# Optimization experiments

Measured on AMD Instinct MI355X. Metric: run time of the kernel, lower is better.

Reference implementation:

```python
import jax, jax.numpy as jnp
import numpy as np

NUM_HEADS = 8
EPS = 1e-12  # torch F.normalize default eps


def conv1x1(x, w):
    # x: [b,c,h,w], w: [o,c]
    return jnp.einsum('bchw,oc->bohw', x, w)


def dwconv3x3(x, w):
    # depthwise 3x3, w: [c,1,3,3]
    return jax.lax.conv_general_dilated(
        x, w, window_strides=(1, 1), padding=((1, 1), (1, 1)),
        dimension_numbers=('NCHW', 'OIHW', 'NCHW'),
        feature_group_count=x.shape[1])


def l2norm(x):
    n = jnp.sqrt(jnp.sum(x * x, axis=-1, keepdims=True))
    return x / jnp.maximum(n, EPS)


def channel_attn(q, k, v, temperature, b, c, h, w):
    hd = c // NUM_HEADS
    q = l2norm(q.reshape(b, NUM_HEADS, hd, h * w))
    k = l2norm(k.reshape(b, NUM_HEADS, hd, h * w))
    v = v.reshape(b, NUM_HEADS, hd, h * w)
    attn = jnp.einsum('bndl,bnel->bnde', q, k) * temperature  # [b,nh,hd,hd]
    attn = jax.nn.softmax(attn, axis=-1)
    out = jnp.einsum('bnde,bnel->bndl', attn, v)
    return out.reshape(b, c, h, w)


def fdfp(x, w1, w2, h, w):
    xf = jnp.fft.rfft2(x, norm='ortho')  # over last two axes
    xfreq = jnp.concatenate([xf.real, xf.imag], axis=1)
    xfreq = conv1x1(xfreq, w1)
    xfreq = jax.nn.gelu(xfreq, approximate=False)
    xfreq = conv1x1(xfreq, w2)
    c2 = xfreq.shape[1] // 2
    xc = jax.lax.complex(xfreq[:, :c2], xfreq[:, c2:])
    return jnp.fft.irfft2(xc, s=(h, w), norm='ortho')


def setup_inputs() -> dict:
    key = jax.random.key(0)
    ks = jax.random.split(key, 10)
    dim = 192
    b, h, w = 4, 128, 128
    s = 0.05
    return {
        'x': jax.random.normal(ks[0], (b, dim, h, w), jnp.float32),
        'w_qkv1': jax.random.normal(ks[1], (3 * dim, dim), jnp.float32) * s,
        'w_qkv1_dw': jax.random.normal(ks[2], (3 * dim, 1, 3, 3), jnp.float32) * s,
        'w_proj1': jax.random.normal(ks[3], (dim, dim), jnp.float32) * s,
        'w_fdfp1': jax.random.normal(ks[4], (2 * dim, 2 * dim), jnp.float32) * s,
        'w_fdfp2': jax.random.normal(ks[5], (2 * dim, 2 * dim), jnp.float32) * s,
        'w_kv2': jax.random.normal(ks[6], (2 * dim, dim), jnp.float32) * s,
        'w_kv2_dw': jax.random.normal(ks[7], (2 * dim, 1, 3, 3), jnp.float32) * s,
        'w_proj2': jax.random.normal(ks[8], (dim, dim), jnp.float32) * s,
        'temperature': jnp.ones((NUM_HEADS, 1, 1), jnp.float32),
    }


def reference(x, w_qkv1, w_qkv1_dw, w_proj1, w_fdfp1, w_fdfp2,
              w_kv2, w_kv2_dw, w_proj2, temperature):
    b, c, h, w = x.shape
    # Stage 1: spatial-domain transposed (channel) attention
    qkv1 = dwconv3x3(conv1x1(x, w_qkv1), w_qkv1_dw)
    q1, k1, v1 = jnp.split(qkv1, 3, axis=1)
    out1 = channel_attn(q1, k1, v1, temperature, b, c, h, w)
    out1 = conv1x1(out1, w_proj1)
    # Stage 2: frequency-domain query, spatial K/V from stage-1 output
    q2 = fdfp(x, w_fdfp1, w_fdfp2, h, w)
    kv2 = dwconv3x3(conv1x1(out1, w_kv2), w_kv2_dw)
    k2, v2 = jnp.split(kv2, 2, axis=1)
    out2 = channel_attn(q2, k2, v2, temperature, b, c, h, w)
    out2 = conv1x1(out2, w_proj2)
    return out2
```

## Files before the change

### kernel.cpp

```cpp
#include <hip/hip_runtime.h>
#include <math.h>

typedef _Float16 half_t;
typedef half_t h8v __attribute__((ext_vector_type(8)));
typedef half_t h4v __attribute__((ext_vector_type(4)));
typedef float f32x4 __attribute__((ext_vector_type(4)));

namespace {
constexpr int DIMC = 192;
constexpr int NB = 4;
constexpr int HH = 128, WW = 128;
constexpr int HW = HH * WW;
constexpr int NH = 8, HD = 24;
constexpr int FP = 80;
constexpr long LT_PART = 128L * 192 * FP;
constexpr long LT_B    = 2 * LT_PART;
constexpr long LT_ROW  = 192L * FP;
constexpr long XB  = 192L * HW;
constexpr long CB0 = 0;
constexpr long CB1 = 15728640;
constexpr long OFF_T1 = 37748736;
constexpr long OFF_Q2 = 50331648;
constexpr long OFF_S  = 62914560;
constexpr long OFF_KT = 0;
constexpr long OFF_KF = 25165824;
constexpr long OFF_O2 = 0;
constexpr int  GSL = 64;
constexpr long SM_INVQ1 = OFF_S;
constexpr long SM_INVK1 = OFF_S + 768;
constexpr long SM_INVQ2 = OFF_S + 1536;
constexpr long SM_INVK2 = OFF_S + 2304;
constexpr long SM_ATT   = OFF_S + 3072;
constexpr long H0       = OFF_S + 168960;
constexpr long H_WQKV = H0;
constexpr long H_WF   = H0 + 55296;
constexpr long H_W1   = H0 + 92160;
constexpr long H_W2   = H0 + 165888;
constexpr long H_PRJ  = H0 + 239616;
constexpr long H_B2   = H0 + 258048;
constexpr long H_B3   = H0 + 290816;
constexpr long H_B1T  = H0 + 323584;
constexpr long H_B4T  = H0 + 333824;
constexpr float PI2 = 6.283185307179586476f;
}

__global__ void cvt16_k(const float* __restrict__ in, half_t* __restrict__ o, int n) {
    int i = blockIdx.x * 256 + threadIdx.x;
    if (i < n) o[i] = (half_t)in[i];
}
__global__ void initB1t_k(half_t* __restrict__ B) {
    int idx = blockIdx.x * 256 + threadIdx.x;
    if (idx >= 160 * 128) return;
    int j = idx / 128, k = idx % 128;
    float v = 0.f;
    if (j < 65) v = cosf(PI2 * ((k * j) & 127) / 128.f) * (1.f / 128.f);
    else if (j >= 80 && j < 145) v = -sinf(PI2 * ((k * (j - 80)) & 127) / 128.f) * (1.f / 128.f);
    B[idx] = (half_t)v;
}
__global__ void initB2h_k(half_t* __restrict__ B) {
    int idx = blockIdx.x * 256 + threadIdx.x;
    int m = idx >> 8, cin = idx & 255;
    int pd = m >> 7, ky = m & 127;
    int ps = cin >> 7, y = cin & 127;
    float c, s; sincosf(PI2 * ((ky * y) & 127) / 128.f, &s, &c);
    float v = (pd == 0) ? (ps == 0 ? c : s) : (ps == 0 ? -s : c);
    B[idx] = (half_t)v;
}
__global__ void initB3h_k(half_t* __restrict__ B) {
    int idx = blockIdx.x * 256 + threadIdx.x;
    int m = idx >> 8, cin = idx & 255;
    int pd = m >> 7, y = m & 127;
    int ps = cin >> 7, ky = cin & 127;
    float c, s; sincosf(PI2 * ((y * ky) & 127) / 128.f, &s, &c);
    float v = (pd == 0) ? (ps == 0 ? c : -s) : (ps == 0 ? s : c);
    B[idx] = (half_t)v;
}
__global__ void initB4t_k(half_t* __restrict__ B) {
    int idx = blockIdx.x * 256 + threadIdx.x;
    if (idx >= 128 * 160) return;
    int j = idx / 160, k = idx % 160;
    float v = 0.f;
    if (k < 80) {
        if (k == 0) v = 1.f / 128.f;
        else if (k < 64) v = 2.f * cosf(PI2 * ((k * j) & 127) / 128.f) / 128.f;
        else if (k == 64) v = cosf(PI2 * ((64 * j) & 127) / 128.f) / 128.f;
    } else {
        int kx = k - 80;
        if (kx >= 1 && kx < 64) v = -2.f * sinf(PI2 * ((kx * j) & 127) / 128.f) / 128.f;
    }
    B[idx] = (half_t)v;
}
__global__ void fusew_k(const float* __restrict__ wkv, const float* __restrict__ wproj,
                        half_t* __restrict__ wf) {
    int o = blockIdx.x, c = threadIdx.x;
    float acc = 0.f;
    for (int m = 0; m < 192; ++m) acc += wkv[o * 192 + m] * wproj[m * 192 + c];
    wf[o * 192 + c] = (half_t)acc;
}

template<int PFOLD, int GELU>
__global__ __launch_bounds__(256) void k2m(
    const half_t* __restrict__ W16, int Cin,
    const float* __restrict__ X, long xBatch, int iSplit, long iLo, long iHi,
    float* __restrict__ out, long oBatch, int oSplit, long oLo, long oHi) {
    __shared__ __align__(16) half_t Wh[64 * 40];
    __shared__ __align__(16) half_t Xh[256 * 40];
    const int t = threadIdx.x;
    const int o0 = blockIdx.x * 64;
    const long p0 = (long)blockIdx.y * 256;
    const long xb = (long)blockIdx.z * xBatch;
    const long ob = (long)blockIdx.z * oBatch;
    const int lane = t & 63, wv = t >> 6;
    const int fr = lane & 15, fg = lane >> 4;
    const int so = t >> 2, scg = (t & 3) * 8;
    f32x4 acc[4][4];
#pragma unroll
    for (int m = 0; m < 4; ++m)
#pragma unroll
        for (int n = 0; n < 4; ++n) acc[m][n] = {0.f, 0.f, 0.f, 0.f};
    long pa;
    {
        long p = p0 + t;
        if (PFOLD) { long q = p / 80; pa = q * LT_ROW + (p - q * 80); } else pa = p;
    }
    for (int k0 = 0; k0 < Cin; k0 += 32) {
        __syncthreads();
        *(h8v*)&Wh[so * 40 + scg] =
            *(const h8v*)(W16 + (long)(o0 + so) * Cin + k0 + scg);
#pragma unroll
        for (int s = 0; s < 2; ++s) {
            int cb = k0 + s * 16;
            long rb = (cb < iSplit) ? (long)cb * iLo : (long)(cb - iSplit) * iLo + iHi;
            const float* g = X + xb + rb + pa;
            float v[16];
#pragma unroll
            for (int j = 0; j < 16; ++j) v[j] = g[(long)j * iLo];
            h8v h0, h1;
#pragma unroll
            for (int j = 0; j < 8; ++j) { h0[j] = (half_t)v[j]; h1[j] = (half_t)v[8 + j]; }
            *(h8v*)&Xh[t * 40 + s * 16] = h0;
            *(h8v*)&Xh[t * 40 + s * 16 + 8] = h1;
        }
        __syncthreads();
        h8v a[4], bb[4];
#pragma unroll
        for (int m = 0; m < 4; ++m) a[m] = *(const h8v*)&Wh[(m * 16 + fr) * 40 + fg * 8];
#pragma unroll
        for (int n = 0; n < 4; ++n) bb[n] = *(const h8v*)&Xh[(wv * 64 + n * 16 + fr) * 40 + fg * 8];
#pragma unroll
        for (int m = 0; m < 4; ++m)
#pragma unroll
            for (int n = 0; n < 4; ++n)
                acc[m][n] = __builtin_amdgcn_mfma_f32_16x16x32_f16(a[m], bb[n], acc[m][n], 0, 0, 0);
    }
    long pe[4];
#pragma unroll
    for (int n = 0; n < 4; ++n) {
        long p = p0 + wv * 64 + n * 16 + fr;
        if (PFOLD) { long q = p / 80; pe[n] = q * LT_ROW + (p - q * 80); } else pe[n] = p;
    }
#pragma unroll
    for (int m = 0; m < 4; ++m)
#pragma unroll
        for (int i = 0; i < 4; ++i) {
            int o = o0 + m * 16 + fg * 4 + i;
            long oadr = ob + ((o < oSplit) ? (long)o * oLo : (long)(o - oSplit) * oLo + oHi);
#pragma unroll
            for (int n = 0; n < 4; ++n) {
                float v = acc[m][n][i];
                if (GELU) v = 0.5f * v * (1.f + erff(v * 0.70710678118654752f));
                out[oadr + pe[n]] = v;
            }
        }
}

__global__ __launch_bounds__(256) void k2big(
    const half_t* __restrict__ B16,
    const float* __restrict__ X, float* __restrict__ out) {
    __shared__ __align__(16) half_t Xh[8 * 64 * 40];
    const int t = threadIdx.x;
    const long p0 = (long)blockIdx.x * 64;
    const long xb = (long)blockIdx.y * LT_B;
    const int lane = t & 63, wv = t >> 6;
    const int fr = lane & 15, fg = lane >> 4;
    {
        const int sp = t & 63;
        const int c0 = t >> 6;
        const float* gp = X + xb + p0 + sp;
#pragma unroll 8
        for (int j = 0; j < 64; ++j) {
            int ci = c0 + j * 4;
            long rb = (ci < 128) ? (long)ci * LT_ROW : (long)(ci - 128) * LT_ROW + LT_PART;
            Xh[((ci >> 5) * 64 + sp) * 40 + (ci & 31)] = (half_t)gp[rb];
        }
    }
    __syncthreads();
    f32x4 acc[4][4];
#pragma unroll
    for (int m = 0; m < 4; ++m)
#pragma unroll
        for (int n = 0; n < 4; ++n) acc[m][n] = {0.f, 0.f, 0.f, 0.f};
    for (int k0 = 0; k0 < 256; k0 += 32) {
        const int s = k0 >> 5;
        h8v a[4], bb[4];
#pragma unroll
        for (int m = 0; m < 4; ++m)
            a[m] = *(const h8v*)(B16 + (long)(wv * 64 + m * 16 + fr) * 256 + k0 + fg * 8);
#pragma unroll
        for (int n = 0; n < 4; ++n)
            bb[n] = *(const h8v*)&Xh[(s * 64 + n * 16 + fr) * 40 + fg * 8];
#pragma unroll
        for (int m = 0; m < 4; ++m)
#pragma unroll
            for (int n = 0; n < 4; ++n)
                acc[m][n] = __builtin_amdgcn_mfma_f32_16x16x32_f16(a[m], bb[n], acc[m][n], 0, 0, 0);
    }
#pragma unroll
    for (int m = 0; m < 4; ++m)
#pragma unroll
        for (int i = 0; i < 4; ++i) {
            int o = wv * 64 + m * 16 + fg * 4 + i;
            long oadr = xb + ((o < 128) ? (long)o * LT_ROW : (long)(o - 128) * LT_ROW + LT_PART);
#pragma unroll
            for (int n = 0; n < 4; ++n)
                out[oadr + p0 + n * 16 + fr] = acc[m][n][i];
        }
}

__global__ __launch_bounds__(512) void kff(
    const half_t* __restrict__ W1, const half_t* __restrict__ W2,
    const float* __restrict__ X, float* __restrict__ out) {
    __shared__ __align__(16) half_t Wh[384 * 40];
    __shared__ __align__(16) half_t Xh[64 * 40];
    __shared__ __align__(16) half_t Yh[64 * 392];
    const int t = threadIdx.x;
    const long p0 = (long)blockIdx.x * 64;
    const long xb = (long)blockIdx.y * LT_B;
    const int lane = t & 63, wv = t >> 6;
    const int fr = lane & 15, fg = lane >> 4;
    const int sp = t & 63;
    const int skb = (t >> 6) * 4;
    long pa;
    { long p = p0 + sp; long q = p / 80; pa = q * LT_ROW + (p - q * 80); }
    f32x4 acc[3][4];
#pragma unroll
    for (int m = 0; m < 3; ++m)
#pragma unroll
        for (int n = 0; n < 4; ++n) acc[m][n] = {0.f, 0.f, 0.f, 0.f};

    for (int k0 = 0; k0 < 384; k0 += 32) {
        __syncthreads();
#pragma unroll
        for (int r = 0; r < 3; ++r) {
            int task = t + r * 512;
            int o = task >> 2, kg = (task & 3) * 8;
            *(h8v*)&Wh[o * 40 + kg] = *(const h8v*)(W1 + (long)o * 384 + k0 + kg);
        }
        {
            int c0 = k0 + skb;
            long rb = (c0 < 192) ? (long)c0 * 80 : (long)(c0 - 192) * 80 + LT_PART;
            const float* g = X + xb + rb + pa;
            h4v h;
#pragma unroll
            for (int j = 0; j < 4; ++j) h[j] = (half_t)g[(long)j * 80];
            *(h4v*)&Xh[sp * 40 + skb] = h;
        }
        __syncthreads();
        h8v a[3], bb[4];
#pragma unroll
        for (int m = 0; m < 3; ++m) a[m] = *(const h8v*)&Wh[(wv * 48 + m * 16 + fr) * 40 + fg * 8];
#pragma unroll
        for (int n = 0; n < 4; ++n) bb[n] = *(const h8v*)&Xh[(n * 16 + fr) * 40 + fg * 8];
#pragma unroll
        for (int m = 0; m < 3; ++m)
#pragma unroll
            for (int n = 0; n < 4; ++n)
                acc[m][n] = __builtin_amdgcn_mfma_f32_16x16x32_f16(a[m], bb[n], acc[m][n], 0, 0, 0);
    }
#pragma unroll
    for (int m = 0; m < 3; ++m)
#pragma unroll
        for (int n = 0; n < 4; ++n) {
            int o4 = wv * 48 + m * 16 + fg * 4;
            int p = n * 16 + fr;
            h4v h;
#pragma unroll
            for (int i = 0; i < 4; ++i) {
                float v = acc[m][n][i];
                v = 0.5f * v * (1.f + erff(v * 0.70710678118654752f));
                h[i] = (half_t)v;
            }
            *(h4v*)&Yh[p * 392 + o4] = h;
        }
#pragma unroll
    for (int m = 0; m < 3; ++m)
#pragma unroll
        for (int n = 0; n < 4; ++n) acc[m][n] = {0.f, 0.f, 0.f, 0.f};

    for (int k0 = 0; k0 < 384; k0 += 32) {
        __syncthreads();
#pragma unroll
        for (int r = 0; r < 3; ++r) {
            int task = t + r * 512;
            int o = task >> 2, kg = (task & 3) * 8;
            *(h8v*)&Wh[o * 40 + kg] = *(const h8v*)(W2 + (long)o * 384 + k0 + kg);
        }
        __syncthreads();
        h8v a[3], bb[4];
#pragma unroll
        for (int m = 0; m < 3; ++m) a[m] = *(const h8v*)&Wh[(wv * 48 + m * 16 + fr) * 40 + fg * 8];
#pragma unroll
        for (int n = 0; n < 4; ++n) bb[n] = *(const h8v*)&Yh[(n * 16 + fr) * 392 + k0 + fg * 8];
#pragma unroll
        for (int m = 0; m < 3; ++m)
#pragma unroll
            for (int n = 0; n < 4; ++n)
                acc[m][n] = __builtin_amdgcn_mfma_f32_16x16x32_f16(a[m], bb[n], acc[m][n], 0, 0, 0);
    }
    long pe[4];
#pragma unroll
    for (int n = 0; n < 4; ++n) {
        long p = p0 + n * 16 + fr;
        long q = p / 80; pe[n] = q * LT_ROW + (p - q * 80);
    }
#pragma unroll
    for (int m = 0; m < 3; ++m)
#pragma unroll
        for (int i = 0; i < 4; ++i) {
            int o = wv * 48 + m * 16 + fg * 4 + i;
            long oadr = xb + ((o < 192) ? (long)o * 80 : (long)(o - 192) * 80 + LT_PART);
#pragma unroll
            for (int n = 0; n < 4; ++n) out[oadr + pe[n]] = acc[m][n][i];
        }
}

template<int NF, int NORM>
__global__ __launch_bounds__(256) void k1m(
    const float* __restrict__ A, long aBatch, long aC, long aRow, int aSplit, long aHiOff, int K,
    const uint* __restrict__ Bt32,
    float* __restrict__ out, long oBatch, long oC, long oRow, int oSplit, long oHiOff,
    float* __restrict__ inv) {
    __shared__ __align__(16) half_t Ah[128 * 40];
    __shared__ __align__(16) half_t Bh[160 * 40];
    const int t = threadIdx.x;
    const long ab = (long)blockIdx.z * aBatch + (long)blockIdx.x * aC;
    const long ob = (long)blockIdx.z * oBatch + (long)blockIdx.x * oC;
    const int N = NF * 32;
    const int lane = t & 63, wv = t >> 6;
    const int wm = wv >> 1, wn = wv & 1;
    const int fr = lane & 15, fg = lane >> 4;
    const int sr = t >> 1, shalf = t & 1;
    const int Kw = K >> 1;
    f32x4 acc[4][NF];
#pragma unroll
    for (int m = 0; m < 4; ++m)
#pragma unroll
        for (int n = 0; n < NF; ++n) acc[m][n] = {0.f, 0.f, 0.f, 0.f};
    for (int k0 = 0; k0 < K; k0 += 32) {
        __syncthreads();
        {
            int cb = k0 + shalf * 16;
            long rb = (cb < aSplit) ? (long)cb : (long)(cb - aSplit) + aHiOff;
            const float* g = A + ab + (long)sr * aRow + rb;
            float4 v0 = *(const float4*)g;
            float4 v1 = *(const float4*)(g + 4);
            float4 v2 = *(const float4*)(g + 8);
            float4 v3 = *(const float4*)(g + 12);
            h8v h0, h1;
            h0[0] = (half_t)v0.x; h0[1] = (half_t)v0.y; h0[2] = (half_t)v0.z; h0[3] = (half_t)v0.w;
            h0[4] = (half_t)v1.x; h0[5] = (half_t)v1.y; h0[6] = (half_t)v1.z; h0[7] = (half_t)v1.w;
            h1[0] = (half_t)v2.x; h1[1] = (half_t)v2.y; h1[2] = (half_t)v2.z; h1[3] = (half_t)v2.w;
            h1[4] = (half_t)v3.x; h1[5] = (half_t)v3.y; h1[6] = (half_t)v3.z; h1[7] = (half_t)v3.w;
            *(h8v*)&Ah[sr * 40 + shalf * 16] = h0;
            *(h8v*)&Ah[sr * 40 + shalf * 16 + 8] = h1;
        }
        for (int j = t; j < N * 16; j += 256) {
            int n = j >> 4, kw = j & 15;
            *(uint*)&Bh[n * 40 + kw * 2] = Bt32[(long)n * Kw + (k0 >> 1) + kw];
        }
        __syncthreads();
        h8v a[4], bb[NF];
#pragma unroll
        for (int m = 0; m < 4; ++m) a[m] = *(const h8v*)&Ah[(wm * 64 + m * 16 + fr) * 40 + fg * 8];
#pragma unroll
        for (int n = 0; n < NF; ++n) bb[n] = *(const h8v*)&Bh[(wn * NF * 16 + n * 16 + fr) * 40 + fg * 8];
#pragma unroll
        for (int m = 0; m < 4; ++m)
#pragma unroll
            for (int n = 0; n < NF; ++n)
                acc[m][n] = __builtin_amdgcn_mfma_f32_16x16x32_f16(a[m], bb[n], acc[m][n], 0, 0, 0);
    }
#pragma unroll
    for (int m = 0; m < 4; ++m)
#pragma unroll
        for (int i = 0; i < 4; ++i) {
            int r = wm * 64 + m * 16 + fg * 4 + i;
            float* orow = out + ob + (long)r * oRow;
#pragma unroll
            for (int n = 0; n < NF; ++n) {
                int j = wn * NF * 16 + n * 16 + fr;
                long jm = (j < oSplit) ? (long)j : (long)(j - oSplit) + oHiOff;
                orow[jm] = acc[m][n][i];
            }
        }
    if (NORM) {
        float ss = 0.f;
#pragma unroll
        for (int m = 0; m < 4; ++m)
#pragma unroll
            for (int n = 0; n < NF; ++n)
#pragma unroll
                for (int i = 0; i < 4; ++i) ss += acc[m][n][i] * acc[m][n][i];
        __syncthreads();
        float* red = (float*)Ah;
        red[t] = ss;
        __syncthreads();
        for (int st = 128; st > 0; st >>= 1) {
            if (t < st) red[t] += red[t + st];
            __syncthreads();
        }
        if (t == 0) inv[(long)blockIdx.z * 192 + blockIdx.x] = 1.f / fmaxf(sqrtf(red[0]), 1e-12f);
    }
}

__global__ __launch_bounds__(256) void dw3_k(
    const float* __restrict__ in, long inBatch,
    const float* __restrict__ w9,
    float* __restrict__ out, long outBatch,
    int normCnt, float* __restrict__ inv) {
    const int c = blockIdx.x, b = blockIdx.y;
    const int t = threadIdx.x;
    const float* ip = in + (long)b * inBatch + (long)c * HW;
    float* op = out + (long)b * outBatch + (long)c * HW;
    const float* wp = w9 + c * 9;
    const float w0 = wp[0], w1 = wp[1], w2 = wp[2];
    const float w3 = wp[3], w4 = wp[4], w5 = wp[5];
    const float w6 = wp[6], w7 = wp[7], w8 = wp[8];
    const int tx = t & 31;
    const int x0 = tx * 4;
    const int y0 = (t >> 5) * 16;
    const bool lx = (tx > 0), rx = (tx < 31);
    float Ar[6], Br[6], Cr[6];
#define LOADROW(Y, R) do { \
        const float* _p = ip + (Y) * 128 + x0; \
        float4 _v = *(const float4*)_p; \
        R[1] = _v.x; R[2] = _v.y; R[3] = _v.z; R[4] = _v.w; \
        R[0] = lx ? _p[-1] : 0.f; \
        R[5] = rx ? _p[4] : 0.f; } while (0)
    if (y0 == 0) { Ar[0]=Ar[1]=Ar[2]=Ar[3]=Ar[4]=Ar[5]=0.f; }
    else LOADROW(y0 - 1, Ar);
    LOADROW(y0, Br);
    float ss = 0.f;
#pragma unroll
    for (int i = 0; i < 16; ++i) {
        int y = y0 + i;
        if (y + 1 < 128) { LOADROW(y + 1, Cr); }
        else { Cr[0]=Cr[1]=Cr[2]=Cr[3]=Cr[4]=Cr[5]=0.f; }
        float o0 = Ar[0]*w0 + Ar[1]*w1 + Ar[2]*w2
                 + Br[0]*w3 + Br[1]*w4 + Br[2]*w5
                 + Cr[0]*w6 + Cr[1]*w7 + Cr[2]*w8;
        float o1 = Ar[1]*w0 + Ar[2]*w1 + Ar[3]*w2
                 + Br[1]*w3 + Br[2]*w4 + Br[3]*w5
                 + Cr[1]*w6 + Cr[2]*w7 + Cr[3]*w8;
        float o2 = Ar[2]*w0 + Ar[3]*w1 + Ar[4]*w2
                 + Br[2]*w3 + Br[3]*w4 + Br[4]*w5
                 + Cr[2]*w6 + Cr[3]*w7 + Cr[4]*w8;
        float o3 = Ar[3]*w0 + Ar[4]*w1 + Ar[5]*w2
                 + Br[3]*w3 + Br[4]*w4 + Br[5]*w5
                 + Cr[3]*w6 + Cr[4]*w7 + Cr[5]*w8;
        *(float4*)(op + y * 128 + x0) = make_float4(o0, o1, o2, o3);
        ss += o0*o0 + o1*o1 + o2*o2 + o3*o3;
#pragma unroll
        for (int j = 0; j < 6; ++j) { Ar[j] = Br[j]; Br[j] = Cr[j]; }
    }
#undef LOADROW
    if (normCnt > 0 && c < normCnt) {
        __shared__ float red[256];
        red[t] = ss;
        __syncthreads();
        for (int st = 128; st > 0; st >>= 1) {
            if (t < st) red[t] += red[t + st];
            __syncthreads();
        }
        if (t == 0) inv[(long)b * 192 + c] = 1.f / fmaxf(sqrtf(red[0]), 1e-12f);
    }
}

__global__ __launch_bounds__(576) void gramf_k(
    const float* __restrict__ q, long qB,
    const float* __restrict__ k, long kB,
    float* __restrict__ gp) {
    __shared__ float qs[HD][260];
    __shared__ float ks[HD][260];
    const int bn = blockIdx.x, ls = blockIdx.y;
    const int b = bn >> 3, n = bn & 7;
    const int t = threadIdx.x;
    const int l0 = ls * 256;
    const float* qp = q + (long)b * qB + (long)(n * HD) * HW + l0;
    const float* kp = k + (long)b * kB + (long)(n * HD) * HW + l0;
    for (int idx = t; idx < HD * 64; idx += 576) {
        int row = idx >> 6, c4 = (idx & 63) * 4;
        *(float4*)&qs[row][c4] = *(const float4*)(qp + (long)row * HW + c4);
        *(float4*)&ks[row][c4] = *(const float4*)(kp + (long)row * HW + c4);
    }
    __syncthreads();
    const int d = t / 24, e = t - d * 24;
    float acc = 0.f;
#pragma unroll 8
    for (int j = 0; j < 256; j += 4) {
        float4 a = *(const float4*)&qs[d][j];
        float4 bb = *(const float4*)&ks[e][j];
        acc += a.x * bb.x + a.y * bb.y + a.z * bb.z + a.w * bb.w;
    }
    gp[((long)bn * 576 + t) * GSL + ls] = acc;
}

__global__ __launch_bounds__(256) void softmax_k(
    const float* __restrict__ gp, const float* __restrict__ invq,
    const float* __restrict__ invk, const float* __restrict__ temp,
    float* __restrict__ attn) {
    int bn = blockIdx.x;
    int b = bn >> 3, n = bn & 7;
    int t = threadIdx.x;
    __shared__ float sums[576];
    for (int idx = t; idx < 576; idx += 256) {
        const float* g = gp + ((long)bn * 576 + idx) * GSL;
        float s = 0.f;
        for (int i = 0; i < GSL; i += 4) {
            float4 v = *(const float4*)(g + i);
            s += v.x + v.y + v.z + v.w;
        }
        sums[idx] = s;
    }
    __syncthreads();
    int d = t;
    if (d >= HD) return;
    float tt = temp[n];
    float iq = invq[b * 192 + n * HD + d];
    float row[HD];
#pragma unroll
    for (int e = 0; e < HD; ++e)
        row[e] = sums[d * HD + e] * iq * invk[b * 192 + n * HD + e] * tt;
    float m = row[0];
#pragma unroll
    for (int e = 1; e < HD; ++e) m = fmaxf(m, row[e]);
    float ssum = 0.f;
#pragma unroll
    for (int e = 0; e < HD; ++e) { row[e] = expf(row[e] - m); ssum += row[e]; }
    float is = 1.f / ssum;
#pragma unroll
    for (int e = 0; e < HD; ++e) attn[(long)bn * 576 + d * HD + e] = row[e] * is;
}

__global__ void attnapply_k(const float* __restrict__ attn, const float* __restrict__ v,
                            long vB, float* __restrict__ out, long outB) {
    int p = blockIdx.x * 256 + threadIdx.x;
    int bn = blockIdx.y;
    int b = bn >> 3, n = bn & 7;
    __shared__ float a[576];
    for (int i = threadIdx.x; i < 576; i += 256) a[i] = attn[(long)bn * 576 + i];
    __syncthreads();
    const float* vp = v + (long)b * vB + (long)(n * HD) * HW + p;
    float acc[HD];
#pragma unroll
    for (int d = 0; d < HD; ++d) acc[d] = 0.f;
    for (int e = 0; e < HD; ++e) {
        float vv = vp[(long)e * HW];
#pragma unroll
        for (int d = 0; d < HD; ++d) acc[d] += a[d * HD + e] * vv;
    }
    float* op = out + (long)b * outB + (long)(n * HD) * HW + p;
#pragma unroll
    for (int d = 0; d < HD; ++d) op[(long)d * HW] = acc[d];
}

extern "C" void kernel_launch(void* const* d_in, const int* in_sizes, int n_in,
                              void* d_out, int out_size, void* d_ws, size_t ws_size,
                              hipStream_t stream) {
    const float* x        = (const float*)d_in[0];
    const float* w_qkv1   = (const float*)d_in[1];
    const float* w_qkv1dw = (const float*)d_in[2];
    const float* w_proj1  = (const float*)d_in[3];
    const float* w_fdfp1  = (const float*)d_in[4];
    const float* w_fdfp2  = (const float*)d_in[5];
    const float* w_kv2    = (const float*)d_in[6];
    const float* w_kv2dw  = (const float*)d_in[7];
    const float* w_proj2  = (const float*)d_in[8];
    const float* temp     = (const float*)d_in[9];
    float* out = (float*)d_out;
    float* ws  = (float*)d_ws;
    dim3 blk(256);
    const int BIG = 1 << 20;

    cvt16_k<<<432, blk, 0, stream>>>(w_qkv1, (half_t*)(ws + H_WQKV), 110592);
    cvt16_k<<<576, blk, 0, stream>>>(w_fdfp1, (half_t*)(ws + H_W1), 147456);
    cvt16_k<<<576, blk, 0, stream>>>(w_fdfp2, (half_t*)(ws + H_W2), 147456);
    cvt16_k<<<144, blk, 0, stream>>>(w_proj2, (half_t*)(ws + H_PRJ), 36864);
    initB1t_k<<<80, blk, 0, stream>>>((half_t*)(ws + H_B1T));
    initB2h_k<<<256, blk, 0, stream>>>((half_t*)(ws + H_B2));
    initB3h_k<<<256, blk, 0, stream>>>((half_t*)(ws + H_B3));
    initB4t_k<<<80, blk, 0, stream>>>((half_t*)(ws + H_B4T));
    fusew_k<<<384, 192, 0, stream>>>(w_kv2, w_proj1, (half_t*)(ws + H_WF));

    k1m<5, 0><<<dim3(192, 1, 4), blk, 0, stream>>>(
        x, XB, (long)HW, 128L, BIG, 0L, 128,
        (const uint*)(ws + H_B1T),
        ws + CB0, LT_B, (long)FP, LT_ROW, 80, LT_PART, nullptr);
    k2big<<<dim3(240, 4), blk, 0, stream>>>(
        (const half_t*)(ws + H_B2), ws + CB0, ws + CB1);
    kff<<<dim3(160, 4), 512, 0, stream>>>(
        (const half_t*)(ws + H_W1), (const half_t*)(ws + H_W2),
        ws + CB1, ws + CB0);
    k2big<<<dim3(240, 4), blk, 0, stream>>>(
        (const half_t*)(ws + H_B3), ws + CB0, ws + CB1);
    k1m<4, 1><<<dim3(192, 1, 4), blk, 0, stream>>>(
        ws + CB1, LT_B, (long)FP, LT_ROW, 80, LT_PART, 160,
        (const uint*)(ws + H_B4T),
        ws + OFF_Q2, XB, (long)HW, 128L, BIG, 0L, ws + SM_INVQ2);

    for (int ch = 0; ch < 3; ++ch) {
        k2m<0, 0><<<dim3(3, 64, 4), blk, 0, stream>>>(
            (const half_t*)(ws + H_WQKV) + (long)ch * 192 * 192, 192,
            x, XB, BIG, (long)HW, 0L,
            ws + OFF_T1, XB, BIG, (long)HW, 0L);
        dw3_k<<<dim3(192, 4), blk, 0, stream>>>(
            ws + OFF_T1, XB, w_qkv1dw + ch * 192 * 9,
            ws + (long)ch * 192 * HW, (long)576 * HW,
            ch == 2 ? 0 : 192,
            ch == 0 ? ws + SM_INVQ1 : ws + SM_INVK1);
    }
    gramf_k<<<dim3(32, GSL), 576, 0, stream>>>(
        ws, (long)576 * HW, ws + (long)192 * HW, (long)576 * HW, ws + OFF_T1);
    softmax_k<<<32, blk, 0, stream>>>(ws + OFF_T1, ws + SM_INVQ1, ws + SM_INVK1, temp, ws + SM_ATT);
    attnapply_k<<<dim3(64, 32), blk, 0, stream>>>(
        ws + SM_ATT, ws + (long)384 * HW, (long)576 * HW, ws + OFF_T1, XB);

    k2m<0, 0><<<dim3(6, 64, 4), blk, 0, stream>>>(
        (const half_t*)(ws + H_WF), 192,
        ws + OFF_T1, XB, BIG, (long)HW, 0L,
        ws + OFF_KT, (long)384 * HW, BIG, (long)HW, 0L);
    dw3_k<<<dim3(384, 4), blk, 0, stream>>>(
        ws + OFF_KT, (long)384 * HW, w_kv2dw, ws + OFF_KF, (long)384 * HW,
        192, ws + SM_INVK2);

    gramf_k<<<dim3(32, GSL), 576, 0, stream>>>(
        ws + OFF_Q2, XB, ws + OFF_KF, (long)384 * HW, ws + OFF_KT);
    softmax_k<<<32, blk, 0, stream>>>(ws + OFF_KT, ws + SM_INVQ2, ws + SM_INVK2, temp, ws + SM_ATT);
    attnapply_k<<<dim3(64, 32), blk, 0, stream>>>(
        ws + SM_ATT, ws + OFF_KF + (long)192 * HW, (long)384 * HW, ws + OFF_O2, XB);
    k2m<0, 0><<<dim3(3, 64, 4), blk, 0, stream>>>(
        (const half_t*)(ws + H_PRJ), 192,
        ws + OFF_O2, XB, BIG, (long)HW, 0L,
        out, XB, BIG, (long)HW, 0L);
}
```

Measured before the change: 654.1 us.

## Stage FFT-domain input tile once in LDS and read MLP weights from global

The frequency-domain MLP kernel now loads the whole 64-pixel by 384-channel input tile into shared memory up front and reuses that same buffer for the GELU intermediate. The weight operands are read straight from global memory (L2/L1 cached) instead of being staged through LDS on every k-step. This removes the per-iteration barrier pairs and cuts LDS from about 81 KB to about 61 KB, which may allow more blocks per CU. In exchange, weight fragments come from uncoalesced global h8v loads, and no prefetch overlaps them with the MFMAs.

```diff
diff --git a/kernel.cpp b/kernel.cpp
--- a/kernel.cpp
+++ b/kernel.cpp
@@ -227,56 +227,55 @@
         }
 }
 
-__global__ __launch_bounds__(512) void kff(
+__global__ __launch_bounds__(512) void kff4(
     const half_t* __restrict__ W1, const half_t* __restrict__ W2,
     const float* __restrict__ X, float* __restrict__ out) {
-    __shared__ __align__(16) half_t Wh[384 * 40];
-    __shared__ __align__(16) half_t Xh[64 * 40];
-    __shared__ __align__(16) half_t Yh[64 * 392];
+    __shared__ __align__(16) half_t S[12 * 64 * 40];
     const int t = threadIdx.x;
     const long p0 = (long)blockIdx.x * 64;
     const long xb = (long)blockIdx.y * LT_B;
     const int lane = t & 63, wv = t >> 6;
     const int fr = lane & 15, fg = lane >> 4;
-    const int sp = t & 63;
-    const int skb = (t >> 6) * 4;
-    long pa;
-    { long p = p0 + sp; long q = p / 80; pa = q * LT_ROW + (p - q * 80); }
+    {
+        const int sp = t & 63;
+        const int g = t >> 6;
+        long pa; { long p = p0 + sp; long q = p / 80; pa = q * LT_ROW + (p - q * 80); }
+        const float* gp = X + xb + pa;
+#pragma unroll
+        for (int ch = 0; ch < 12; ++ch) {
+            int ci0 = ch * 32 + g * 4;
+            h4v h;
+#pragma unroll
+            for (int j = 0; j < 4; ++j) {
+                int ci = ci0 + j;
+                long rb = (ci < 192) ? (long)ci * 80 : (long)(ci - 192) * 80 + LT_PART;
+                h[j] = (half_t)gp[rb];
+            }
+            *(h4v*)&S[(ch * 64 + sp) * 40 + g * 4] = h;
+        }
+    }
+    __syncthreads();
     f32x4 acc[3][4];
 #pragma unroll
     for (int m = 0; m < 3; ++m)
 #pragma unroll
         for (int n = 0; n < 4; ++n) acc[m][n] = {0.f, 0.f, 0.f, 0.f};
-
     for (int k0 = 0; k0 < 384; k0 += 32) {
-        __syncthreads();
-#pragma unroll
-        for (int r = 0; r < 3; ++r) {
-            int task = t + r * 512;
-            int o = task >> 2, kg = (task & 3) * 8;
-            *(h8v*)&Wh[o * 40 + kg] = *(const h8v*)(W1 + (long)o * 384 + k0 + kg);
-        }
-        {
-            int c0 = k0 + skb;
-            long rb = (c0 < 192) ? (long)c0 * 80 : (long)(c0 - 192) * 80 + LT_PART;
-            const float* g = X + xb + rb + pa;
-            h4v h;
-#pragma unroll
-            for (int j = 0; j < 4; ++j) h[j] = (half_t)g[(long)j * 80];
-            *(h4v*)&Xh[sp * 40 + skb] = h;
-        }
-        __syncthreads();
+        const int s = k0 >> 5;
         h8v a[3], bb[4];
 #pragma unroll
-        for (int m = 0; m < 3; ++m) a[m] = *(const h8v*)&Wh[(wv * 48 + m * 16 + fr) * 40 + fg * 8];
-#pragma unroll
-        for (int n = 0; n < 4; ++n) bb[n] = *(const h8v*)&Xh[(n * 16 + fr) * 40 + fg * 8];
+        for (int m = 0; m < 3; ++m)
+            a[m] = *(const h8v*)(W1 + (long)(wv * 48 + m * 16 + fr) * 384 + k0 + fg * 8);
+#pragma unroll
+        for (int n = 0; n < 4; ++n)
+            bb[n] = *(const h8v*)&S[(s * 64 + n * 16 + fr) * 40 + fg * 8];
 #pragma unroll
         for (int m = 0; m < 3; ++m)
 #pragma unroll
             for (int n = 0; n < 4; ++n)
                 acc[m][n] = __builtin_amdgcn_mfma_f32_16x16x32_f16(a[m], bb[n], acc[m][n], 0, 0, 0);
     }
+    __syncthreads();
 #pragma unroll
     for (int m = 0; m < 3; ++m)
 #pragma unroll
@@ -290,27 +289,22 @@
                 v = 0.5f * v * (1.f + erff(v * 0.70710678118654752f));
                 h[i] = (half_t)v;
             }
-            *(h4v*)&Yh[p * 392 + o4] = h;
+            *(h4v*)&S[((o4 >> 5) * 64 + p) * 40 + (o4 & 31)] = h;
         }
 #pragma unroll
     for (int m = 0; m < 3; ++m)
 #pragma unroll
         for (int n = 0; n < 4; ++n) acc[m][n] = {0.f, 0.f, 0.f, 0.f};
-
+    __syncthreads();
     for (int k0 = 0; k0 < 384; k0 += 32) {
-        __syncthreads();
-#pragma unroll
-        for (int r = 0; r < 3; ++r) {
-            int task = t + r * 512;
-            int o = task >> 2, kg = (task & 3) * 8;
-            *(h8v*)&Wh[o * 40 + kg] = *(const h8v*)(W2 + (long)o * 384 + k0 + kg);
-        }
-        __syncthreads();
+        const int s = k0 >> 5;
         h8v a[3], bb[4];
 #pragma unroll
-        for (int m = 0; m < 3; ++m) a[m] = *(const h8v*)&Wh[(wv * 48 + m * 16 + fr) * 40 + fg * 8];
-#pragma unroll
-        for (int n = 0; n < 4; ++n) bb[n] = *(const h8v*)&Yh[(n * 16 + fr) * 392 + k0 + fg * 8];
+        for (int m = 0; m < 3; ++m)
+            a[m] = *(const h8v*)(W2 + (long)(wv * 48 + m * 16 + fr) * 384 + k0 + fg * 8);
+#pragma unroll
+        for (int n = 0; n < 4; ++n)
+            bb[n] = *(const h8v*)&S[(s * 64 + n * 16 + fr) * 40 + fg * 8];
 #pragma unroll
         for (int m = 0; m < 3; ++m)
 #pragma unroll
@@ -608,7 +602,7 @@
         ws + CB0, LT_B, (long)FP, LT_ROW, 80, LT_PART, nullptr);
     k2big<<<dim3(240, 4), blk, 0, stream>>>(
         (const half_t*)(ws + H_B2), ws + CB0, ws + CB1);
-    kff<<<dim3(160, 4), 512, 0, stream>>>(
+    kff4<<<dim3(160, 4), 512, 0, stream>>>(
         (const half_t*)(ws + H_W1), (const half_t*)(ws + H_W2),
         ws + CB1, ws + CB0);
     k2big<<<dim3(240, 4), blk, 0, stream>>>(
```

New measurement: 632.6 us. 1.03x faster.
